# Performance work log

Measured on AMD Instinct MI355X. Metric: run time of the kernel, lower is better.

## Reference

```python
import jax, jax.numpy as jnp
import numpy as np

B, S, DIN, D, H = 32, 2048, 1024, 512, 8
NC, NM = 19, 10


def _mha(q_in, kv, Wq, bq, Wk, bk, Wv, bv, Wo, bo, add_mask):
    # q_in: [B,S,D]; kv: [K,D] (shared across batch); add_mask: [B,S,K] additive logit bias
    Bq, Sq, Dm = q_in.shape
    dh = Dm // H
    q = (q_in @ Wq + bq).reshape(Bq, Sq, H, dh)
    k = (kv @ Wk + bk).reshape(-1, H, dh)
    v = (kv @ Wv + bv).reshape(-1, H, dh)
    logits = jnp.einsum('bshd,khd->bhsk', q, k) / jnp.sqrt(jnp.float32(dh))
    attn = jax.nn.softmax(logits + add_mask[:, None, :, :], axis=-1)  # [B,H,S,K]
    out = jnp.einsum('bhsk,khd->bshd', attn, v).reshape(Bq, Sq, Dm)
    return out @ Wo + bo


def setup_inputs() -> dict:
    key = jax.random.key(0)
    ks = jax.random.split(key, 32)
    s = 0.02
    p = lambda i, shape: jax.random.normal(ks[i], shape, jnp.float32) * s
    z = lambda: jnp.zeros((D,), jnp.float32)
    return {
        'embeddings': jax.random.normal(ks[0], (B, S, DIN), jnp.float32),
        'embeddings_mask': jax.random.randint(ks[1], (B, S), 0, 2, jnp.int32),
        'post_mask': jax.random.randint(ks[2], (B, S), 0, 2, jnp.int32),
        'frame_mask': jax.random.randint(ks[3], (B, S), 0, 2, jnp.int32),
        'cultural_mask': jax.random.randint(ks[4], (B, NC), 0, 2, jnp.int32),
        'moral_mask': jax.random.randint(ks[5], (B, NM), 0, 2, jnp.int32),
        'W_lin': p(6, (DIN, D)), 'b_lin': z(),
        'cultural_table': p(7, (NC, D)), 'moral_table': p(8, (NM, D)),
        'c_Wq': p(9, (D, D)), 'c_bq': z(), 'c_Wk': p(10, (D, D)), 'c_bk': z(),
        'c_Wv': p(11, (D, D)), 'c_bv': z(), 'c_Wo': p(12, (D, D)), 'c_bo': z(),
        'm_Wq': p(13, (D, D)), 'm_bq': z(), 'm_Wk': p(14, (D, D)), 'm_bk': z(),
        'm_Wv': p(15, (D, D)), 'm_bv': z(), 'm_Wo': p(16, (D, D)), 'm_bo': z(),
    }


def reference(embeddings, embeddings_mask, post_mask, frame_mask, cultural_mask, moral_mask,
              W_lin, b_lin, cultural_table, moral_table,
              c_Wq, c_bq, c_Wk, c_bk, c_Wv, c_bv, c_Wo, c_bo,
              m_Wq, m_bq, m_Wk, m_bk, m_Wv, m_bv, m_Wo, m_bo):
    x = embeddings @ W_lin + b_lin  # [B,S,D]
    em = embeddings_mask.astype(jnp.float32)
    pm = em * post_mask.astype(jnp.float32)   # combined post mask [B,S]
    fm = em * frame_mask.astype(jnp.float32)  # combined frame mask [B,S]
    cm = cultural_mask.astype(jnp.float32)    # [B,NC]
    mm = moral_mask.astype(jnp.float32)       # [B,NM]
    cw = (c_Wq, c_bq, c_Wk, c_bk, c_Wv, c_bv, c_Wo, c_bo)
    mw = (m_Wq, m_bq, m_Wk, m_bk, m_Wv, m_bv, m_Wo, m_bo)
    # cultural branch: two stacked cross-attentions, float masks are ADDED to logits
    fc = _mha(x, cultural_table, *cw, fm[:, :, None] + cm[:, None, :])
    pc = _mha(fc, cultural_table, *cw, pm[:, :, None] + cm[:, None, :])
    post_cultural = pc.sum(axis=1) / pm.sum(axis=1, keepdims=True)
    # moral branch
    fmo = _mha(x, moral_table, *mw, fm[:, :, None] + mm[:, None, :])
    pmo = _mha(fmo, moral_table, *mw, pm[:, :, None] + mm[:, None, :])
    post_moral = pmo.sum(axis=1) / pm.sum(axis=1, keepdims=True)
    pooled = post_cultural - post_moral
    return post_cultural, pooled
```

## Files before the change

### kernel.cpp

```cpp
#include <hip/hip_runtime.h>
#include <math.h>

typedef __bf16 bf16;
typedef __bf16 bf16x8 __attribute__((ext_vector_type(8)));
typedef float floatx4 __attribute__((ext_vector_type(4)));

#define S_LEN 2048
#define BATCH 32
#define NHEAD 8
#define KC 19
#define KM 10
#define HKC 152
#define HKM 80
#define NTOT 232
#define NPAD 256

__global__ __launch_bounds__(256) void prep1(
    const int* __restrict__ em, const int* __restrict__ pmask,
    const int* __restrict__ cmask, const int* __restrict__ mmask,
    const float* __restrict__ ctab, const float* __restrict__ mtab,
    const float* __restrict__ cWk, const float* __restrict__ cbk,
    const float* __restrict__ cWv, const float* __restrict__ cbv,
    const float* __restrict__ mWk, const float* __restrict__ mbk,
    const float* __restrict__ mWv, const float* __restrict__ mbv,
    float* __restrict__ P, float* __restrict__ A2, float* __restrict__ mb,
    float* __restrict__ k1c, float* __restrict__ v1c,
    float* __restrict__ k1m, float* __restrict__ v1m,
    bf16* __restrict__ GT, bf16* __restrict__ Bt,
    float* __restrict__ c1, float* __restrict__ c2)
{
    __shared__ float smem[512];
    const int blk = blockIdx.x, tid = threadIdx.x;

    if (blk < 32) {
        int* red = (int*)smem;
        int b = blk;
        int s = 0;
        for (int i = tid; i < S_LEN; i += 256) s += em[b*S_LEN+i] * pmask[b*S_LEN+i];
        red[tid] = s; __syncthreads();
        for (int o = 128; o; o >>= 1) { if (tid < o) red[tid] += red[tid+o]; __syncthreads(); }
        if (tid == 0) P[b] = (float)red[0];
        float v = 0.f;
        if (tid < HKC) v = (float)cmask[b*KC + (tid % KC)];
        else if (tid < NTOT) v = (float)mmask[b*KM + ((tid - HKC) % KM)];
        mb[b*NPAD + tid] = v;
        A2[b*NPAD + tid] = 0.f;
    } else if (blk < 61) {
        int r = blk - 32;
        const float* T;  const float* Wk; const float* bk; const float* Wv; const float* bv;
        float* k1; float* v1; int row;
        if (r < KC) { T = ctab; Wk = cWk; bk = cbk; Wv = cWv; bv = cbv; k1 = k1c; v1 = v1c; row = r; }
        else        { T = mtab; Wk = mWk; bk = mbk; Wv = mWv; bv = mbv; k1 = k1m; v1 = v1m; row = r - KC; }
        for (int i = tid; i < 512; i += 256) smem[i] = T[row*512+i];
        __syncthreads();
        for (int j = tid; j < 512; j += 256) {
            float sk = bk[j], sv = bv[j];
            for (int d = 0; d < 512; d++) { float t = smem[d]; sk += t*Wk[d*512+j]; sv += t*Wv[d*512+j]; }
            k1[row*512+j] = sk; v1[row*512+j] = sv;
        }
    } else {
        int z = blk - 61;
        for (int i = tid; i < 16384; i += 256) GT[z*16384 + i] = (bf16)0.f;
        for (int i = tid; i < 6144; i += 256) Bt[(size_t)NTOT*1024 + z*6144 + i] = (bf16)0.f;
        if (z == 0) { c1[tid] = 0.f; c2[tid] = 0.f; }
    }
}

__global__ __launch_bounds__(256) void prep2(
    const float* __restrict__ cWq, const float* __restrict__ mWq,
    const float* __restrict__ k1c, const float* __restrict__ v1c,
    const float* __restrict__ k1m, const float* __restrict__ v1m,
    const float* __restrict__ cWo, const float* __restrict__ mWo,
    float* __restrict__ MqTd, float* __restrict__ W2)
{
    __shared__ float smem[15872];
    const int blk = blockIdx.x, tid = threadIdx.x;

    if (blk < 512) {
        int D = blk;
        for (int i = tid; i < 9728; i += 256) smem[i] = k1c[i];
        for (int i = tid; i < 5120; i += 256) smem[9728+i] = k1m[i];
        for (int i = tid; i < 512; i += 256) {
            smem[14848+i] = cWq[(size_t)D*512+i];
            smem[15360+i] = mWq[(size_t)D*512+i];
        }
        __syncthreads();
        if (tid < HKC) {
            int h = tid / KC, k = tid % KC;
            const float* kr = smem + k*512 + h*64;
            float mq = 0.f;
            #pragma unroll 16
            for (int d = 0; d < 64; d++) mq += smem[14848 + h*64 + d] * kr[d];
            MqTd[D*NPAD + tid] = mq;
        }
        if (tid < HKM) {
            int h = tid / KM, k = tid % KM;
            const float* kr = smem + 9728 + k*512 + h*64;
            float mq = 0.f;
            #pragma unroll 16
            for (int d = 0; d < 64; d++) mq += smem[15360 + h*64 + d] * kr[d];
            MqTd[D*NPAD + HKC + tid] = mq;
        }
    } else {
        int n = blk - 512;
        const float* v1; const float* Wo; int h, k;
        if (n < HKC) { v1 = v1c; Wo = cWo; h = n / KC; k = n % KC; }
        else         { v1 = v1m; Wo = mWo; h = (n-HKC) / KM; k = (n-HKC) % KM; }
        if (tid < 64) smem[tid] = v1[k*512 + h*64 + tid];
        __syncthreads();
        for (int j = tid; j < 512; j += 256) {
            float s = 0.f;
            #pragma unroll 16
            for (int d = 0; d < 64; d++) s += smem[d] * Wo[(size_t)(h*64+d)*512 + j];
            W2[(size_t)n*512 + j] = s;
        }
    }
}

__global__ __launch_bounds__(256) void prep3(
    const float* __restrict__ W_lin, const float* __restrict__ b_lin,
    const float* __restrict__ MqTd, const float* __restrict__ W2,
    const float* __restrict__ k1c, const float* __restrict__ k1m,
    const float* __restrict__ cbq, const float* __restrict__ mbq,
    const float* __restrict__ cbo, const float* __restrict__ mbo,
    bf16* __restrict__ Bt, bf16* __restrict__ GT, float* __restrict__ c1, float* __restrict__ c2)
{
    __shared__ float smem[4096];
    const int blk = blockIdx.x, tid = threadIdx.x;

    if (blk < NTOT) {
        int n = blk;
        for (int i = tid; i < 512; i += 256) smem[i] = W2[(size_t)n*512 + i];
        __syncthreads();
        if (n < HKC) {
            for (int np = tid; np < HKC; np += 256) {
                float s = 0.f;
                for (int t = 0; t < 512; t++) s += smem[t] * MqTd[t*NPAD + np];
                GT[(size_t)np*NPAD + n] = (bf16)(0.125f*s);
            }
        } else {
            for (int np = tid; np < HKM; np += 256) {
                float s = 0.f;
                for (int t = 0; t < 512; t++) s += smem[t] * MqTd[t*NPAD + HKC + np];
                GT[(size_t)(HKC+np)*NPAD + n] = (bf16)(0.125f*s);
            }
        }
    } else if (blk < 360) {
        int D0 = (blk - NTOT) * 8;
        for (int i = tid; i < 4096; i += 256)
            smem[i] = W_lin[(size_t)(D0 + (i >> 9))*512 + (i & 511)];
        __syncthreads();
        if (tid < NTOT) {
            float acc[8] = {};
            for (int d = 0; d < 512; d++) {
                float m = MqTd[d*NPAD + tid];
                #pragma unroll
                for (int r = 0; r < 8; r++) acc[r] += smem[r*512 + d] * m;
            }
            #pragma unroll
            for (int r = 0; r < 8; r++)
                Bt[(size_t)tid*1024 + D0 + r] = (bf16)(0.125f*acc[r]);
        }
    } else {
        for (int i = tid; i < 512; i += 256) {
            smem[i] = b_lin[i];
            smem[512+i] = cbo[i];
            smem[1024+i] = mbo[i];
        }
        __syncthreads();
        if (tid < NTOT) {
            bool cult = tid < HKC;
            const float* bo_s = cult ? (smem+512) : (smem+1024);
            float sA = 0.f, sB = 0.f;
            for (int D = 0; D < 512; D++) {
                float m = MqTd[D*NPAD + tid];
                sA += smem[D]*m;
                sB += bo_s[D]*m;
            }
            float skq = 0.f;
            if (cult) {
                int h = tid / KC, k = tid % KC;
                for (int d = 0; d < 64; d++) skq += cbq[h*64+d] * k1c[k*512 + h*64 + d];
            } else {
                int nm = tid - HKC, h = nm / KM, k = nm % KM;
                for (int d = 0; d < 64; d++) skq += mbq[h*64+d] * k1m[k*512 + h*64 + d];
            }
            c1[tid] = 0.125f*(sA + skq);
            c2[tid] = 0.125f*(sB + skq);
        }
    }
}

__global__ __launch_bounds__(256, 2) void g1_kernel(const float* __restrict__ emb,
                                                    const bf16* __restrict__ Bt,
                                                    const float* __restrict__ c1,
                                                    const float* __restrict__ mb,
                                                    bf16* __restrict__ av1)
{
    __shared__ union UU {
        struct { bf16 As[128*40]; bf16 Bs[256*40]; } s;
        bf16 Ls[128*264];
    } u;
    __shared__ float bias[256];
    const int tid = threadIdx.x;
    const int m0 = blockIdx.x*128, b = blockIdx.x >> 4;
    bias[tid] = c1[tid] + mb[b*NPAD + tid];
    const int wave = tid >> 6, lane = tid & 63, lr = lane & 15, kg = lane >> 4;
    floatx4 acc[8][4] = {};
    const int arow = tid >> 1, acol = (tid & 1)*16;
    const float* ap = emb + (size_t)(m0 + arow)*1024 + acol;
    bf16* asw = u.s.As + arow*40 + acol;
    const bf16* bp = Bt + (size_t)tid*1024;
    bf16* bsw = u.s.Bs + tid*40;
    const bf16* afp = u.s.As + lr*40 + kg*8;
    const bf16* bfp = u.s.Bs + (wave*64 + lr)*40 + kg*8;

    for (int k0 = 0; k0 < 1024; k0 += 32) {
        float4 f0 = *(const float4*)(ap + k0);
        float4 f1 = *(const float4*)(ap + k0 + 4);
        float4 f2 = *(const float4*)(ap + k0 + 8);
        float4 f3 = *(const float4*)(ap + k0 + 12);
        uint4 b0 = *(const uint4*)(bp + k0);
        uint4 b1 = *(const uint4*)(bp + k0 + 8);
        uint4 b2 = *(const uint4*)(bp + k0 + 16);
        uint4 b3 = *(const uint4*)(bp + k0 + 24);
        __syncthreads();
        bf16x8 p0, p1;
        p0[0]=(bf16)f0.x; p0[1]=(bf16)f0.y; p0[2]=(bf16)f0.z; p0[3]=(bf16)f0.w;
        p0[4]=(bf16)f1.x; p0[5]=(bf16)f1.y; p0[6]=(bf16)f1.z; p0[7]=(bf16)f1.w;
        p1[0]=(bf16)f2.x; p1[1]=(bf16)f2.y; p1[2]=(bf16)f2.z; p1[3]=(bf16)f2.w;
        p1[4]=(bf16)f3.x; p1[5]=(bf16)f3.y; p1[6]=(bf16)f3.z; p1[7]=(bf16)f3.w;
        *(bf16x8*)asw = p0; *(bf16x8*)(asw + 8) = p1;
        *(uint4*)bsw = b0; *(uint4*)(bsw + 8) = b1; *(uint4*)(bsw + 16) = b2; *(uint4*)(bsw + 24) = b3;
        __syncthreads();
        bf16x8 af[8], bfr[4];
        #pragma unroll
        for (int mi = 0; mi < 8; mi++) af[mi] = *(const bf16x8*)(afp + mi*16*40);
        #pragma unroll
        for (int nt = 0; nt < 4; nt++) bfr[nt] = *(const bf16x8*)(bfp + nt*16*40);
        #pragma unroll
        for (int mi = 0; mi < 8; mi++)
            #pragma unroll
            for (int nt = 0; nt < 4; nt++)
                acc[mi][nt] = __builtin_amdgcn_mfma_f32_16x16x32_bf16(af[mi], bfr[nt], acc[mi][nt], 0, 0, 0);
    }
    __syncthreads();
    #pragma unroll
    for (int nt = 0; nt < 4; nt++) {
        int col = wave*64 + nt*16 + lr;
        float bb = bias[col];
        #pragma unroll
        for (int mi = 0; mi < 8; mi++) {
            int row = mi*16 + kg*4;
            #pragma unroll
            for (int r = 0; r < 4; r++)
                u.Ls[(row + r)*264 + col] = (bf16)(acc[mi][nt][r] + bb);
        }
    }
    __syncthreads();
    {
        int row = tid & 127;
        bf16* Lr = u.Ls + row*264;
        if (tid < 128) {
            for (int h = 0; h < NHEAD; h++) {
                float lv[KC]; float m = -1e30f;
                #pragma unroll
                for (int j = 0; j < KC; j++) { lv[j] = (float)Lr[h*KC + j]; m = fmaxf(m, lv[j]); }
                float s = 0.f;
                #pragma unroll
                for (int j = 0; j < KC; j++) { lv[j] = __expf(lv[j] - m); s += lv[j]; }
                float inv = 1.f / s;
                #pragma unroll
                for (int j = 0; j < KC; j++) Lr[h*KC + j] = (bf16)(lv[j]*inv);
            }
        } else {
            for (int h = 0; h < NHEAD; h++) {
                float lv[KM]; float m = -1e30f;
                #pragma unroll
                for (int j = 0; j < KM; j++) { lv[j] = (float)Lr[HKC + h*KM + j]; m = fmaxf(m, lv[j]); }
                float s = 0.f;
                #pragma unroll
                for (int j = 0; j < KM; j++) { lv[j] = __expf(lv[j] - m); s += lv[j]; }
                float inv = 1.f / s;
                #pragma unroll
                for (int j = 0; j < KM; j++) Lr[HKC + h*KM + j] = (bf16)(lv[j]*inv);
            }
            for (int c = NTOT; c < NPAD; c++) Lr[c] = (bf16)0.f;
        }
    }
    __syncthreads();
    for (int c = tid; c < 4096; c += 256) {
        int row = c >> 5, c8 = (c & 31)*8;
        *(uint4*)(av1 + (size_t)(m0 + row)*NPAD + c8) = *(const uint4*)(u.Ls + row*264 + c8);
    }
}

__global__ __launch_bounds__(256, 2) void g2_kernel(const bf16* __restrict__ av1,
                                                    const bf16* __restrict__ GT,
                                                    const float* __restrict__ c2,
                                                    const float* __restrict__ mb,
                                                    float* __restrict__ A2)
{
    __shared__ union UU {
        struct { bf16 As[128*40]; bf16 Bs[256*40]; } s;
        bf16 Ls[128*264];
    } u;
    __shared__ float bias[256];
    const int tid = threadIdx.x;
    const int m0 = blockIdx.x*128, b = blockIdx.x >> 4;
    bias[tid] = c2[tid] + mb[b*NPAD + tid];
    const int wave = tid >> 6, lane = tid & 63, lr = lane & 15, kg = lane >> 4;
    floatx4 acc[8][4] = {};
    const int arow = tid >> 1, acol = (tid & 1)*16;
    const bf16* ap = av1 + (size_t)(m0 + arow)*NPAD + acol;
    bf16* asw = u.s.As + arow*40 + acol;
    const bf16* bp = GT + (size_t)tid*NPAD;
    bf16* bsw = u.s.Bs + tid*40;
    const bf16* afp = u.s.As + lr*40 + kg*8;
    const bf16* bfp = u.s.Bs + (wave*64 + lr)*40 + kg*8;

    for (int k0 = 0; k0 < 256; k0 += 32) {
        uint4 a0 = *(const uint4*)(ap + k0);
        uint4 a1 = *(const uint4*)(ap + k0 + 8);
        uint4 b0 = *(const uint4*)(bp + k0);
        uint4 b1 = *(const uint4*)(bp + k0 + 8);
        uint4 b2 = *(const uint4*)(bp + k0 + 16);
        uint4 b3 = *(const uint4*)(bp + k0 + 24);
        __syncthreads();
        *(uint4*)asw = a0; *(uint4*)(asw + 8) = a1;
        *(uint4*)bsw = b0; *(uint4*)(bsw + 8) = b1; *(uint4*)(bsw + 16) = b2; *(uint4*)(bsw + 24) = b3;
        __syncthreads();
        bf16x8 af[8], bfr[4];
        #pragma unroll
        for (int mi = 0; mi < 8; mi++) af[mi] = *(const bf16x8*)(afp + mi*16*40);
        #pragma unroll
        for (int nt = 0; nt < 4; nt++) bfr[nt] = *(const bf16x8*)(bfp + nt*16*40);
        #pragma unroll
        for (int mi = 0; mi < 8; mi++)
            #pragma unroll
            for (int nt = 0; nt < 4; nt++)
                acc[mi][nt] = __builtin_amdgcn_mfma_f32_16x16x32_bf16(af[mi], bfr[nt], acc[mi][nt], 0, 0, 0);
    }
    __syncthreads();
    #pragma unroll
    for (int nt = 0; nt < 4; nt++) {
        int col = wave*64 + nt*16 + lr;
        float bb = bias[col];
        #pragma unroll
        for (int mi = 0; mi < 8; mi++) {
            int row = mi*16 + kg*4;
            #pragma unroll
            for (int r = 0; r < 4; r++)
                u.Ls[(row + r)*264 + col] = (bf16)(acc[mi][nt][r] + bb);
        }
    }
    __syncthreads();
    {
        int row = tid & 127;
        bf16* Lr = u.Ls + row*264;
        if (tid < 128) {
            for (int h = 0; h < NHEAD; h++) {
                float lv[KC]; float m = -1e30f;
                #pragma unroll
                for (int j = 0; j < KC; j++) { lv[j] = (float)Lr[h*KC + j]; m = fmaxf(m, lv[j]); }
                float s = 0.f;
                #pragma unroll
                for (int j = 0; j < KC; j++) { lv[j] = __expf(lv[j] - m); s += lv[j]; }
                float inv = 1.f / s;
                #pragma unroll
                for (int j = 0; j < KC; j++) Lr[h*KC + j] = (bf16)(lv[j]*inv);
            }
        } else {
            for (int h = 0; h < NHEAD; h++) {
                float lv[KM]; float m = -1e30f;
                #pragma unroll
                for (int j = 0; j < KM; j++) { lv[j] = (float)Lr[HKC + h*KM + j]; m = fmaxf(m, lv[j]); }
                float s = 0.f;
                #pragma unroll
                for (int j = 0; j < KM; j++) { lv[j] = __expf(lv[j] - m); s += lv[j]; }
                float inv = 1.f / s;
                #pragma unroll
                for (int j = 0; j < KM; j++) Lr[HKC + h*KM + j] = (bf16)(lv[j]*inv);
            }
        }
    }
    __syncthreads();
    {
        float s = 0.f;
        for (int r = 0; r < 128; r++) s += (float)u.Ls[r*264 + tid];
        if (tid < NTOT) atomicAdd(&A2[b*NPAD + tid], s);
    }
}

__global__ __launch_bounds__(256) void finalize_kernel(const float* __restrict__ A2, const float* __restrict__ W2,
                                                       const float* __restrict__ cbo, const float* __restrict__ mbo,
                                                       const float* __restrict__ P, float* __restrict__ out)
{
    __shared__ float a[NTOT];
    int b = blockIdx.x, tid = threadIdx.x;
    if (tid < NTOT) a[tid] = A2[b*NPAD + tid];
    __syncthreads();
    float invP = 1.f / P[b];
    for (int j = tid; j < 512; j += 256) {
        float pc = 2048.f*cbo[j], pm = 2048.f*mbo[j];
        for (int n = 0; n < HKC; n++) pc += a[n]*W2[n*512 + j];
        for (int n = HKC; n < NTOT; n++) pm += a[n]*W2[n*512 + j];
        out[b*512 + j] = pc*invP;
        out[BATCH*512 + b*512 + j] = (pc - pm)*invP;
    }
}

extern "C" void kernel_launch(void* const* d_in, const int* in_sizes, int n_in,
                              void* d_out, int out_size, void* d_ws, size_t ws_size,
                              hipStream_t stream)
{
    (void)in_sizes; (void)n_in; (void)out_size;
    const float* emb   = (const float*)d_in[0];
    const int* emask   = (const int*)d_in[1];
    const int* pmask   = (const int*)d_in[2];
    const int* cmask   = (const int*)d_in[4];
    const int* mmask   = (const int*)d_in[5];
    const float* W_lin = (const float*)d_in[6];
    const float* b_lin = (const float*)d_in[7];
    const float* ctab  = (const float*)d_in[8];
    const float* mtab  = (const float*)d_in[9];
    const float* cWq = (const float*)d_in[10]; const float* cbq = (const float*)d_in[11];
    const float* cWk = (const float*)d_in[12]; const float* cbk = (const float*)d_in[13];
    const float* cWv = (const float*)d_in[14]; const float* cbv = (const float*)d_in[15];
    const float* cWo = (const float*)d_in[16]; const float* cbo = (const float*)d_in[17];
    const float* mWq = (const float*)d_in[18]; const float* mbq = (const float*)d_in[19];
    const float* mWk = (const float*)d_in[20]; const float* mbk = (const float*)d_in[21];
    const float* mWv = (const float*)d_in[22]; const float* mbv = (const float*)d_in[23];
    const float* mWo = (const float*)d_in[24]; const float* mbo = (const float*)d_in[25];
    float* outp = (float*)d_out;

    if (ws_size < 40000000UL) return;

    char* ws = (char*)d_ws;
    size_t o = 0;
    bf16* av1   = (bf16*)(ws + o); o += (size_t)65536*NPAD*2;
    bf16* Bt    = (bf16*)(ws + o); o += 256*1024*2;
    bf16* GT    = (bf16*)(ws + o); o += NPAD*NPAD*2;
    float* k1c  = (float*)(ws + o); o += KC*512*4;
    float* v1c  = (float*)(ws + o); o += KC*512*4;
    float* k1m  = (float*)(ws + o); o += KM*512*4;
    float* v1m  = (float*)(ws + o); o += KM*512*4;
    float* MqTd = (float*)(ws + o); o += (size_t)512*NPAD*4;
    float* W2   = (float*)(ws + o); o += (size_t)NTOT*512*4;
    float* c1   = (float*)(ws + o); o += NPAD*4;
    float* c2   = (float*)(ws + o); o += NPAD*4;
    float* mbt  = (float*)(ws + o); o += BATCH*NPAD*4;
    float* P    = (float*)(ws + o); o += 128;
    float* A2   = (float*)(ws + o); o += BATCH*NPAD*4;

    dim3 blk(256);

    prep1<<<dim3(65), blk, 0, stream>>>(emask, pmask, cmask, mmask, ctab, mtab,
                                        cWk, cbk, cWv, cbv, mWk, mbk, mWv, mbv,
                                        P, A2, mbt, k1c, v1c, k1m, v1m, GT, Bt, c1, c2);
    prep2<<<dim3(744), blk, 0, stream>>>(cWq, mWq, k1c, v1c, k1m, v1m, cWo, mWo, MqTd, W2);
    prep3<<<dim3(361), blk, 0, stream>>>(W_lin, b_lin, MqTd, W2, k1c, k1m,
                                         cbq, mbq, cbo, mbo, Bt, GT, c1, c2);
    g1_kernel<<<dim3(512), blk, 0, stream>>>(emb, Bt, c1, mbt, av1);
    g2_kernel<<<dim3(512), blk, 0, stream>>>(av1, GT, c2, mbt, A2);
    finalize_kernel<<<dim3(BATCH), blk, 0, stream>>>(A2, W2, cbo, mbo, P, outp);
}
```

Baseline: 645.9 us.

## Fuse both attention GEMM stages into one double-buffered kernel

Merges the first and second logit GEMM+softmax stages into a single kernel, so the intermediate attention probabilities stay in LDS instead of a 32 MB bf16 round-trip through global memory. The first GEMM's K loop becomes double-buffered with register prefetch and one barrier per step. The second GEMM reads its A operand directly from the LDS softmax tile and streams the B fragments (GT) from global into registers. The cost is doubled staging LDS plus extra registers for the second accumulator set, which may pressure occupancy.

```diff
diff --git a/kernel.cpp b/kernel.cpp
--- a/kernel.cpp
+++ b/kernel.cpp
@@ -14,6 +14,14 @@
 #define HKM 80
 #define NTOT 232
 #define NPAD 256
+
+#define BAR() do { \
+    asm volatile("s_waitcnt lgkmcnt(0)" ::: "memory"); \
+    __builtin_amdgcn_s_barrier(); \
+    asm volatile("" ::: "memory"); \
+} while (0)
+
+static __device__ __forceinline__ bf16x8 as_b8(uint4 v) { return __builtin_bit_cast(bf16x8, v); }
 
 __global__ __launch_bounds__(256) void prep1(
     const int* __restrict__ em, const int* __restrict__ pmask,
@@ -191,64 +199,88 @@
     }
 }
 
-__global__ __launch_bounds__(256, 2) void g1_kernel(const float* __restrict__ emb,
-                                                    const bf16* __restrict__ Bt,
-                                                    const float* __restrict__ c1,
-                                                    const float* __restrict__ mb,
-                                                    bf16* __restrict__ av1)
+__global__ __launch_bounds__(256, 2) void g12_kernel(const float* __restrict__ emb,
+                                                     const bf16* __restrict__ Bt,
+                                                     const bf16* __restrict__ GT,
+                                                     const float* __restrict__ c1,
+                                                     const float* __restrict__ c2,
+                                                     const float* __restrict__ mb,
+                                                     float* __restrict__ A2)
 {
     __shared__ union UU {
-        struct { bf16 As[128*40]; bf16 Bs[256*40]; } s;
+        struct { bf16 As[2][128*40]; bf16 Bs[2][256*40]; } s;
         bf16 Ls[128*264];
     } u;
-    __shared__ float bias[256];
+    __shared__ float bias1[256], bias2[256];
     const int tid = threadIdx.x;
     const int m0 = blockIdx.x*128, b = blockIdx.x >> 4;
-    bias[tid] = c1[tid] + mb[b*NPAD + tid];
+    bias1[tid] = c1[tid] + mb[b*NPAD + tid];
+    bias2[tid] = c2[tid] + mb[b*NPAD + tid];
     const int wave = tid >> 6, lane = tid & 63, lr = lane & 15, kg = lane >> 4;
     floatx4 acc[8][4] = {};
     const int arow = tid >> 1, acol = (tid & 1)*16;
     const float* ap = emb + (size_t)(m0 + arow)*1024 + acol;
-    bf16* asw = u.s.As + arow*40 + acol;
     const bf16* bp = Bt + (size_t)tid*1024;
-    bf16* bsw = u.s.Bs + tid*40;
-    const bf16* afp = u.s.As + lr*40 + kg*8;
-    const bf16* bfp = u.s.Bs + (wave*64 + lr)*40 + kg*8;
-
-    for (int k0 = 0; k0 < 1024; k0 += 32) {
-        float4 f0 = *(const float4*)(ap + k0);
-        float4 f1 = *(const float4*)(ap + k0 + 4);
-        float4 f2 = *(const float4*)(ap + k0 + 8);
-        float4 f3 = *(const float4*)(ap + k0 + 12);
-        uint4 b0 = *(const uint4*)(bp + k0);
-        uint4 b1 = *(const uint4*)(bp + k0 + 8);
-        uint4 b2 = *(const uint4*)(bp + k0 + 16);
-        uint4 b3 = *(const uint4*)(bp + k0 + 24);
-        __syncthreads();
+    bf16* asw0 = u.s.As[0] + arow*40 + acol;
+    bf16* asw1 = u.s.As[1] + arow*40 + acol;
+    bf16* bsw0 = u.s.Bs[0] + tid*40;
+    bf16* bsw1 = u.s.Bs[1] + tid*40;
+    const bf16* afp0 = u.s.As[0] + lr*40 + kg*8;
+    const bf16* afp1 = u.s.As[1] + lr*40 + kg*8;
+    const bf16* bfp0 = u.s.Bs[0] + (wave*64 + lr)*40 + kg*8;
+    const bf16* bfp1 = u.s.Bs[1] + (wave*64 + lr)*40 + kg*8;
+
+    float4 fA[4]; uint4 gB[4];
+    auto loads = [&](int k0) {
+        fA[0] = *(const float4*)(ap + k0);     fA[1] = *(const float4*)(ap + k0 + 4);
+        fA[2] = *(const float4*)(ap + k0 + 8); fA[3] = *(const float4*)(ap + k0 + 12);
+        gB[0] = *(const uint4*)(bp + k0);      gB[1] = *(const uint4*)(bp + k0 + 8);
+        gB[2] = *(const uint4*)(bp + k0 + 16); gB[3] = *(const uint4*)(bp + k0 + 24);
+    };
+    auto stage = [&](bf16* asw_, bf16* bsw_) {
         bf16x8 p0, p1;
-        p0[0]=(bf16)f0.x; p0[1]=(bf16)f0.y; p0[2]=(bf16)f0.z; p0[3]=(bf16)f0.w;
-        p0[4]=(bf16)f1.x; p0[5]=(bf16)f1.y; p0[6]=(bf16)f1.z; p0[7]=(bf16)f1.w;
-        p1[0]=(bf16)f2.x; p1[1]=(bf16)f2.y; p1[2]=(bf16)f2.z; p1[3]=(bf16)f2.w;
-        p1[4]=(bf16)f3.x; p1[5]=(bf16)f3.y; p1[6]=(bf16)f3.z; p1[7]=(bf16)f3.w;
-        *(bf16x8*)asw = p0; *(bf16x8*)(asw + 8) = p1;
-        *(uint4*)bsw = b0; *(uint4*)(bsw + 8) = b1; *(uint4*)(bsw + 16) = b2; *(uint4*)(bsw + 24) = b3;
-        __syncthreads();
+        p0[0]=(bf16)fA[0].x; p0[1]=(bf16)fA[0].y; p0[2]=(bf16)fA[0].z; p0[3]=(bf16)fA[0].w;
+        p0[4]=(bf16)fA[1].x; p0[5]=(bf16)fA[1].y; p0[6]=(bf16)fA[1].z; p0[7]=(bf16)fA[1].w;
+        p1[0]=(bf16)fA[2].x; p1[1]=(bf16)fA[2].y; p1[2]=(bf16)fA[2].z; p1[3]=(bf16)fA[2].w;
+        p1[4]=(bf16)fA[3].x; p1[5]=(bf16)fA[3].y; p1[6]=(bf16)fA[3].z; p1[7]=(bf16)fA[3].w;
+        *(bf16x8*)asw_ = p0; *(bf16x8*)(asw_ + 8) = p1;
+        *(uint4*)bsw_ = gB[0]; *(uint4*)(bsw_ + 8) = gB[1];
+        *(uint4*)(bsw_ + 16) = gB[2]; *(uint4*)(bsw_ + 24) = gB[3];
+    };
+    auto fragmfma = [&](const bf16* afp_, const bf16* bfp_) {
         bf16x8 af[8], bfr[4];
         #pragma unroll
-        for (int mi = 0; mi < 8; mi++) af[mi] = *(const bf16x8*)(afp + mi*16*40);
-        #pragma unroll
-        for (int nt = 0; nt < 4; nt++) bfr[nt] = *(const bf16x8*)(bfp + nt*16*40);
+        for (int mi = 0; mi < 8; mi++) af[mi] = *(const bf16x8*)(afp_ + mi*16*40);
+        #pragma unroll
+        for (int nt = 0; nt < 4; nt++) bfr[nt] = *(const bf16x8*)(bfp_ + nt*16*40);
         #pragma unroll
         for (int mi = 0; mi < 8; mi++)
             #pragma unroll
             for (int nt = 0; nt < 4; nt++)
                 acc[mi][nt] = __builtin_amdgcn_mfma_f32_16x16x32_bf16(af[mi], bfr[nt], acc[mi][nt], 0, 0, 0);
-    }
-    __syncthreads();
+    };
+
+    loads(0);
+    stage(asw0, bsw0);
+    loads(32);
+    BAR();
+    #pragma unroll 1
+    for (int t = 0; t < 30; t += 2) {
+        fragmfma(afp0, bfp0); stage(asw1, bsw1); loads((t + 2)*32); BAR();
+        fragmfma(afp1, bfp1); stage(asw0, bsw0); loads((t + 3)*32); BAR();
+    }
+    fragmfma(afp0, bfp0); stage(asw1, bsw1); BAR();
+    fragmfma(afp1, bfp1);
+    const bf16* gt0 = GT + (size_t)(wave*64 + lr)*NPAD + kg*8;
+    uint4 gb[4];
+    #pragma unroll
+    for (int nt = 0; nt < 4; nt++) gb[nt] = *(const uint4*)(gt0 + nt*16*NPAD);
+    BAR();
+
     #pragma unroll
     for (int nt = 0; nt < 4; nt++) {
         int col = wave*64 + nt*16 + lr;
-        float bb = bias[col];
+        float bb = bias1[col];
         #pragma unroll
         for (int mi = 0; mi < 8; mi++) {
             int row = mi*16 + kg*4;
@@ -257,7 +289,7 @@
                 u.Ls[(row + r)*264 + col] = (bf16)(acc[mi][nt][r] + bb);
         }
     }
-    __syncthreads();
+    BAR();
     {
         int row = tid & 127;
         bf16* Lr = u.Ls + row*264;
@@ -288,73 +320,45 @@
             for (int c = NTOT; c < NPAD; c++) Lr[c] = (bf16)0.f;
         }
     }
-    __syncthreads();
-    for (int c = tid; c < 4096; c += 256) {
-        int row = c >> 5, c8 = (c & 31)*8;
-        *(uint4*)(av1 + (size_t)(m0 + row)*NPAD + c8) = *(const uint4*)(u.Ls + row*264 + c8);
-    }
-}
-
-__global__ __launch_bounds__(256, 2) void g2_kernel(const bf16* __restrict__ av1,
-                                                    const bf16* __restrict__ GT,
-                                                    const float* __restrict__ c2,
-                                                    const float* __restrict__ mb,
-                                                    float* __restrict__ A2)
-{
-    __shared__ union UU {
-        struct { bf16 As[128*40]; bf16 Bs[256*40]; } s;
-        bf16 Ls[128*264];
-    } u;
-    __shared__ float bias[256];
-    const int tid = threadIdx.x;
-    const int m0 = blockIdx.x*128, b = blockIdx.x >> 4;
-    bias[tid] = c2[tid] + mb[b*NPAD + tid];
-    const int wave = tid >> 6, lane = tid & 63, lr = lane & 15, kg = lane >> 4;
-    floatx4 acc[8][4] = {};
-    const int arow = tid >> 1, acol = (tid & 1)*16;
-    const bf16* ap = av1 + (size_t)(m0 + arow)*NPAD + acol;
-    bf16* asw = u.s.As + arow*40 + acol;
-    const bf16* bp = GT + (size_t)tid*NPAD;
-    bf16* bsw = u.s.Bs + tid*40;
-    const bf16* afp = u.s.As + lr*40 + kg*8;
-    const bf16* bfp = u.s.Bs + (wave*64 + lr)*40 + kg*8;
-
-    for (int k0 = 0; k0 < 256; k0 += 32) {
-        uint4 a0 = *(const uint4*)(ap + k0);
-        uint4 a1 = *(const uint4*)(ap + k0 + 8);
-        uint4 b0 = *(const uint4*)(bp + k0);
-        uint4 b1 = *(const uint4*)(bp + k0 + 8);
-        uint4 b2 = *(const uint4*)(bp + k0 + 16);
-        uint4 b3 = *(const uint4*)(bp + k0 + 24);
-        __syncthreads();
-        *(uint4*)asw = a0; *(uint4*)(asw + 8) = a1;
-        *(uint4*)bsw = b0; *(uint4*)(bsw + 8) = b1; *(uint4*)(bsw + 16) = b2; *(uint4*)(bsw + 24) = b3;
-        __syncthreads();
-        bf16x8 af[8], bfr[4];
-        #pragma unroll
-        for (int mi = 0; mi < 8; mi++) af[mi] = *(const bf16x8*)(afp + mi*16*40);
-        #pragma unroll
-        for (int nt = 0; nt < 4; nt++) bfr[nt] = *(const bf16x8*)(bfp + nt*16*40);
+    BAR();
+
+    floatx4 acc2[8][4] = {};
+    const bf16* afp3 = u.Ls + lr*264 + kg*8;
+    #pragma unroll
+    for (int t = 0; t < 8; t++) {
+        uint4 gbn[4];
+        if (t < 7) {
+            #pragma unroll
+            for (int nt = 0; nt < 4; nt++) gbn[nt] = *(const uint4*)(gt0 + nt*16*NPAD + (t + 1)*32);
+        }
+        bf16x8 af3[8];
+        #pragma unroll
+        for (int mi = 0; mi < 8; mi++) af3[mi] = *(const bf16x8*)(afp3 + mi*16*264 + t*32);
         #pragma unroll
         for (int mi = 0; mi < 8; mi++)
             #pragma unroll
             for (int nt = 0; nt < 4; nt++)
-                acc[mi][nt] = __builtin_amdgcn_mfma_f32_16x16x32_bf16(af[mi], bfr[nt], acc[mi][nt], 0, 0, 0);
-    }
-    __syncthreads();
+                acc2[mi][nt] = __builtin_amdgcn_mfma_f32_16x16x32_bf16(af3[mi], as_b8(gb[nt]), acc2[mi][nt], 0, 0, 0);
+        if (t < 7) {
+            #pragma unroll
+            for (int nt = 0; nt < 4; nt++) gb[nt] = gbn[nt];
+        }
+    }
+    BAR();
+
     #pragma unroll
     for (int nt = 0; nt < 4; nt++) {
         int col = wave*64 + nt*16 + lr;
-        float bb = bias[col];
+        float bb = bias2[col];
         #pragma unroll
         for (int mi = 0; mi < 8; mi++) {
             int row = mi*16 + kg*4;
             #pragma unroll
             for (int r = 0; r < 4; r++)
-                u.Ls[(row + r)*264 + col] = (bf16)(acc[mi][nt][r] + bb);
-        }
-    }
-    __syncthreads();
+                u.Ls[(row + r)*264 + col] = (bf16)(acc2[mi][nt][r] + bb);
+        }
+    }
+    BAR();
     {
         int row = tid & 127;
         bf16* Lr = u.Ls + row*264;
@@ -384,7 +388,7 @@
             }
         }
     }
-    __syncthreads();
+    BAR();
     {
         float s = 0.f;
         for (int r = 0; r < 128; r++) s += (float)u.Ls[r*264 + tid];
@@ -438,7 +442,6 @@
 
     char* ws = (char*)d_ws;
     size_t o = 0;
-    bf16* av1   = (bf16*)(ws + o); o += (size_t)65536*NPAD*2;
     bf16* Bt    = (bf16*)(ws + o); o += 256*1024*2;
     bf16* GT    = (bf16*)(ws + o); o += NPAD*NPAD*2;
     float* k1c  = (float*)(ws + o); o += KC*512*4;
@@ -461,7 +464,6 @@
     prep2<<<dim3(744), blk, 0, stream>>>(cWq, mWq, k1c, v1c, k1m, v1m, cWo, mWo, MqTd, W2);
     prep3<<<dim3(361), blk, 0, stream>>>(W_lin, b_lin, MqTd, W2, k1c, k1m,
                                          cbq, mbq, cbo, mbo, Bt, GT, c1, c2);
-    g1_kernel<<<dim3(512), blk, 0, stream>>>(emb, Bt, c1, mbt, av1);
-    g2_kernel<<<dim3(512), blk, 0, stream>>>(av1, GT, c2, mbt, A2);
+    g12_kernel<<<dim3(512), blk, 0, stream>>>(emb, Bt, GT, c1, c2, mbt, A2);
     finalize_kernel<<<dim3(BATCH), blk, 0, stream>>>(A2, W2, cbo, mbo, P, outp);
 }
```

After: 678.0 us. 5.0% more time.

## Fuse stage-1 and stage-2 attention GEMMs into one kernel keeping probabilities in LDS

Applied to the files above, without the earlier changes.

Merges g1 and g2 into a single kernel. The first-stage softmax probabilities stay in shared memory and feed the second GEMM directly, with the GT operand read straight from global memory instead of being staged through LDS. This removes the 32 MB bf16 av1 intermediate write and read-back plus one kernel launch. In exchange it keeps a second 128-register accumulator array live and issues uncoalesced per-lane GT loads from global or L2.

```diff
diff --git a/kernel.cpp b/kernel.cpp
--- a/kernel.cpp
+++ b/kernel.cpp
@@ -14,6 +14,8 @@
 #define HKM 80
 #define NTOT 232
 #define NPAD 256
+
+static __device__ __forceinline__ bf16x8 as_b8(uint4 v) { return __builtin_bit_cast(bf16x8, v); }
 
 __global__ __launch_bounds__(256) void prep1(
     const int* __restrict__ em, const int* __restrict__ pmask,
@@ -191,20 +193,23 @@
     }
 }
 
-__global__ __launch_bounds__(256, 2) void g1_kernel(const float* __restrict__ emb,
-                                                    const bf16* __restrict__ Bt,
-                                                    const float* __restrict__ c1,
-                                                    const float* __restrict__ mb,
-                                                    bf16* __restrict__ av1)
+__global__ __launch_bounds__(256, 2) void g12_kernel(const float* __restrict__ emb,
+                                                     const bf16* __restrict__ Bt,
+                                                     const bf16* __restrict__ GT,
+                                                     const float* __restrict__ c1,
+                                                     const float* __restrict__ c2,
+                                                     const float* __restrict__ mb,
+                                                     float* __restrict__ A2)
 {
     __shared__ union UU {
         struct { bf16 As[128*40]; bf16 Bs[256*40]; } s;
         bf16 Ls[128*264];
     } u;
-    __shared__ float bias[256];
+    __shared__ float bias1[256], bias2[256];
     const int tid = threadIdx.x;
     const int m0 = blockIdx.x*128, b = blockIdx.x >> 4;
-    bias[tid] = c1[tid] + mb[b*NPAD + tid];
+    bias1[tid] = c1[tid] + mb[b*NPAD + tid];
+    bias2[tid] = c2[tid] + mb[b*NPAD + tid];
     const int wave = tid >> 6, lane = tid & 63, lr = lane & 15, kg = lane >> 4;
     floatx4 acc[8][4] = {};
     const int arow = tid >> 1, acol = (tid & 1)*16;
@@ -248,7 +253,7 @@
     #pragma unroll
     for (int nt = 0; nt < 4; nt++) {
         int col = wave*64 + nt*16 + lr;
-        float bb = bias[col];
+        float bb = bias1[col];
         #pragma unroll
         for (int mi = 0; mi < 8; mi++) {
             int row = mi*16 + kg*4;
@@ -289,69 +294,37 @@
         }
     }
     __syncthreads();
-    for (int c = tid; c < 4096; c += 256) {
-        int row = c >> 5, c8 = (c & 31)*8;
-        *(uint4*)(av1 + (size_t)(m0 + row)*NPAD + c8) = *(const uint4*)(u.Ls + row*264 + c8);
-    }
-}
-
-__global__ __launch_bounds__(256, 2) void g2_kernel(const bf16* __restrict__ av1,
-                                                    const bf16* __restrict__ GT,
-                                                    const float* __restrict__ c2,
-                                                    const float* __restrict__ mb,
-                                                    float* __restrict__ A2)
-{
-    __shared__ union UU {
-        struct { bf16 As[128*40]; bf16 Bs[256*40]; } s;
-        bf16 Ls[128*264];
-    } u;
-    __shared__ float bias[256];
-    const int tid = threadIdx.x;
-    const int m0 = blockIdx.x*128, b = blockIdx.x >> 4;
-    bias[tid] = c2[tid] + mb[b*NPAD + tid];
-    const int wave = tid >> 6, lane = tid & 63, lr = lane & 15, kg = lane >> 4;
-    floatx4 acc[8][4] = {};
-    const int arow = tid >> 1, acol = (tid & 1)*16;
-    const bf16* ap = av1 + (size_t)(m0 + arow)*NPAD + acol;
-    bf16* asw = u.s.As + arow*40 + acol;
-    const bf16* bp = GT + (size_t)tid*NPAD;
-    bf16* bsw = u.s.Bs + tid*40;
-    const bf16* afp = u.s.As + lr*40 + kg*8;
-    const bf16* bfp = u.s.Bs + (wave*64 + lr)*40 + kg*8;
-
-    for (int k0 = 0; k0 < 256; k0 += 32) {
-        uint4 a0 = *(const uint4*)(ap + k0);
-        uint4 a1 = *(const uint4*)(ap + k0 + 8);
-        uint4 b0 = *(const uint4*)(bp + k0);
-        uint4 b1 = *(const uint4*)(bp + k0 + 8);
-        uint4 b2 = *(const uint4*)(bp + k0 + 16);
-        uint4 b3 = *(const uint4*)(bp + k0 + 24);
-        __syncthreads();
-        *(uint4*)asw = a0; *(uint4*)(asw + 8) = a1;
-        *(uint4*)bsw = b0; *(uint4*)(bsw + 8) = b1; *(uint4*)(bsw + 16) = b2; *(uint4*)(bsw + 24) = b3;
-        __syncthreads();
-        bf16x8 af[8], bfr[4];
-        #pragma unroll
-        for (int mi = 0; mi < 8; mi++) af[mi] = *(const bf16x8*)(afp + mi*16*40);
-        #pragma unroll
-        for (int nt = 0; nt < 4; nt++) bfr[nt] = *(const bf16x8*)(bfp + nt*16*40);
-        #pragma unroll
-        for (int mi = 0; mi < 8; mi++)
-            #pragma unroll
-            for (int nt = 0; nt < 4; nt++)
-                acc[mi][nt] = __builtin_amdgcn_mfma_f32_16x16x32_bf16(af[mi], bfr[nt], acc[mi][nt], 0, 0, 0);
-    }
-    __syncthreads();
+
+    floatx4 acc2[8][4] = {};
+    {
+        const bf16* afp3 = u.Ls + lr*264 + kg*8;
+        const bf16* gt0 = GT + (size_t)(wave*64 + lr)*NPAD + kg*8;
+        #pragma unroll 2
+        for (int t = 0; t < 8; t++) {
+            bf16x8 gbv[4], af3[8];
+            #pragma unroll
+            for (int nt = 0; nt < 4; nt++) gbv[nt] = *(const bf16x8*)(gt0 + nt*16*NPAD + t*32);
+            #pragma unroll
+            for (int mi = 0; mi < 8; mi++) af3[mi] = *(const bf16x8*)(afp3 + mi*16*264 + t*32);
+            #pragma unroll
+            for (int mi = 0; mi < 8; mi++)
+                #pragma unroll
+                for (int nt = 0; nt < 4; nt++)
+                    acc2[mi][nt] = __builtin_amdgcn_mfma_f32_16x16x32_bf16(af3[mi], gbv[nt], acc2[mi][nt], 0, 0, 0);
+        }
+    }
+    __syncthreads();
+
     #pragma unroll
     for (int nt = 0; nt < 4; nt++) {
         int col = wave*64 + nt*16 + lr;
-        float bb = bias[col];
+        float bb = bias2[col];
         #pragma unroll
         for (int mi = 0; mi < 8; mi++) {
             int row = mi*16 + kg*4;
             #pragma unroll
             for (int r = 0; r < 4; r++)
-                u.Ls[(row + r)*264 + col] = (bf16)(acc[mi][nt][r] + bb);
+                u.Ls[(row + r)*264 + col] = (bf16)(acc2[mi][nt][r] + bb);
         }
     }
     __syncthreads();
@@ -438,7 +411,6 @@
 
     char* ws = (char*)d_ws;
     size_t o = 0;
-    bf16* av1   = (bf16*)(ws + o); o += (size_t)65536*NPAD*2;
     bf16* Bt    = (bf16*)(ws + o); o += 256*1024*2;
     bf16* GT    = (bf16*)(ws + o); o += NPAD*NPAD*2;
     float* k1c  = (float*)(ws + o); o += KC*512*4;
@@ -461,7 +433,6 @@
     prep2<<<dim3(744), blk, 0, stream>>>(cWq, mWq, k1c, v1c, k1m, v1m, cWo, mWo, MqTd, W2);
     prep3<<<dim3(361), blk, 0, stream>>>(W_lin, b_lin, MqTd, W2, k1c, k1m,
                                          cbq, mbq, cbo, mbo, Bt, GT, c1, c2);
-    g1_kernel<<<dim3(512), blk, 0, stream>>>(emb, Bt, c1, mbt, av1);
-    g2_kernel<<<dim3(512), blk, 0, stream>>>(av1, GT, c2, mbt, A2);
+    g12_kernel<<<dim3(512), blk, 0, stream>>>(emb, Bt, GT, c1, c2, mbt, A2);
     finalize_kernel<<<dim3(BATCH), blk, 0, stream>>>(A2, W2, cbo, mbo, P, outp);
 }
```

Result: faster. 630.6 us (-2.4%).
